# Kernel tuning notes

Hardware: AMD Instinct MI355X
Metric: run time of the kernel (lower is better)

The kernel has to match this reference:

```python
import jax, jax.numpy as jnp
import numpy as np

EMBED = 2048
HEADS = 16
B, T = 4, 2048


def setup_inputs() -> dict:
    key = jax.random.key(0)
    ks = jax.random.split(key, 8)
    s = 1.0 / np.sqrt(EMBED)
    return {
        "k": jax.random.normal(ks[0], (B, T, EMBED), dtype=jnp.float32),
        "q": jax.random.normal(ks[1], (B, T, EMBED), dtype=jnp.float32),
        "v": jax.random.normal(ks[2], (B, T, EMBED), dtype=jnp.float32),
        "Wk": jax.random.uniform(ks[3], (EMBED, EMBED), jnp.float32, -s, s),
        "Wq": jax.random.uniform(ks[4], (EMBED, EMBED), jnp.float32, -s, s),
        "Wv": jax.random.uniform(ks[5], (EMBED, EMBED), jnp.float32, -s, s),
        "Wo": jax.random.uniform(ks[6], (EMBED, EMBED), jnp.float32, -s, s),
        "bo": jax.random.uniform(ks[7], (EMBED,), jnp.float32, -s, s),
    }


def _split_heads(x):
    b, t, e = x.shape
    # 'b t (h n) -> b h t n'
    return x.reshape(b, t, HEADS, e // HEADS).transpose(0, 2, 1, 3)


def reference(k, q, v, Wk, Wq, Wv, Wo, bo):
    keys = _split_heads(k @ Wk.T)      # [b,h,t,n]
    queries = _split_heads(q @ Wq.T)
    values = _split_heads(v @ Wv.T)
    head_dim = queries.shape[-1]
    scale = 1.0 / jnp.sqrt(jnp.asarray(head_dim, queries.dtype))
    att = jnp.einsum('bhqn,bhkn->bhqk', queries, keys) * scale
    att = jax.nn.softmax(att, axis=-1)
    out = jnp.einsum('bhqk,bhkn->bhqn', att, values)  # [b,h,t,n]
    b, h, t, n = out.shape
    out = out.transpose(0, 2, 1, 3).reshape(b, t, h * n)  # 'b h t n -> b t (h n)'
    return out @ Wo.T + bo
```

## Files before the change

kernel.cpp:

```cpp
#include <hip/hip_runtime.h>


typedef __attribute__((ext_vector_type(4))) float f32x4;
typedef __attribute__((ext_vector_type(2))) float f32x2;
typedef __attribute__((ext_vector_type(8))) __bf16 bf16x8;
typedef __attribute__((ext_vector_type(4))) unsigned int u32x4;
typedef __attribute__((ext_vector_type(8))) unsigned short u16x8;
typedef __attribute__((ext_vector_type(4))) unsigned short u16x4;

#define DEVI static __device__ __forceinline__

DEVI unsigned short f2bf(float f) {
  union { float f; unsigned u; } x; x.f = f;
  unsigned u = x.u;
  return (unsigned short)((u + 0x7fffu + ((u >> 16) & 1u)) >> 16);
}
DEVI unsigned int pack2(float lo, float hi) {
  return (unsigned int)f2bf(lo) | ((unsigned int)f2bf(hi) << 16);
}
DEVI u32x4 pack8(const f32x4 a, const f32x4 b) {
  u32x4 r;
  r[0] = pack2(a[0], a[1]); r[1] = pack2(a[2], a[3]);
  r[2] = pack2(b[0], b[1]); r[3] = pack2(b[2], b[3]);
  return r;
}
DEVI void gload16(const unsigned short* g, unsigned short* l) {
  __builtin_amdgcn_global_load_lds(
      (const __attribute__((address_space(1))) unsigned int*)g,
      (__attribute__((address_space(3))) unsigned int*)l, 16, 0, 0);
}

template <int CTRL> DEVI float dppf(float x) {
  return __builtin_bit_cast(float, __builtin_amdgcn_update_dpp(
      __builtin_bit_cast(int, x), __builtin_bit_cast(int, x), CTRL, 0xF, 0xF, true));
}
DEVI float rowmax16(float x) {
  x = fmaxf(x, dppf<0x121>(x));
  x = fmaxf(x, dppf<0x122>(x));
  x = fmaxf(x, dppf<0x124>(x));
  x = fmaxf(x, dppf<0x128>(x));
  return x;
}
DEVI float rowsum16(float x) {
  x += dppf<0x121>(x);
  x += dppf<0x122>(x);
  x += dppf<0x124>(x);
  x += dppf<0x128>(x);
  return x;
}

__global__ __launch_bounds__(256) void convA(
    const float* __restrict__ q, const float* __restrict__ k,
    const float* __restrict__ v, unsigned short* __restrict__ dst)
{
  const int z = blockIdx.z;
  const float* src = z == 0 ? q : (z == 1 ? k : v);
  unsigned short* d = dst + (size_t)z * 16777216;
  size_t i = ((size_t)blockIdx.x * 256 + threadIdx.x) * 8;
  f32x4 a = *(const f32x4*)(src + i);
  f32x4 b = *(const f32x4*)(src + i + 4);
  *(u32x4*)(d + i) = pack8(a, b);
}

__global__ __launch_bounds__(256) void convW(
    const float* __restrict__ w0, const float* __restrict__ w1,
    const float* __restrict__ w2, const float* __restrict__ w3,
    unsigned short* __restrict__ dst)
{
  const int z = blockIdx.z;
  const float* src = z == 0 ? w0 : (z == 1 ? w1 : (z == 2 ? w2 : w3));
  unsigned short* d = dst + (size_t)z * 4194304;
  size_t i = ((size_t)blockIdx.x * 256 + threadIdx.x) * 8;
  f32x4 a = *(const f32x4*)(src + i);
  f32x4 b = *(const f32x4*)(src + i + 4);
  *(u32x4*)(d + i) = pack8(a, b);
}

#define STG2(gp, lp, tile) do { \
    gload16((gp) + (size_t)(tile) * 64,            (lp)); \
    gload16((gp) + (size_t)(tile) * 64 + 8 * 2048, (lp) + 8 * 64); \
  } while (0)
#define LDA8(bufoff, ksbit) { \
    _Pragma("unroll") for (int m = 0; m < 8; m++) \
      a[m] = *(const bf16x8*)(As + (bufoff) + (aoff[m] ^ (ksbit))); }
#define LDB2(bufoff, ksbit, n0) { \
    b0 = *(const bf16x8*)(Bs + (bufoff) + (boff[n0] ^ (ksbit))); \
    b1 = *(const bf16x8*)(Bs + (bufoff) + (boff[(n0) + 1] ^ (ksbit))); }
#define MM2(n0) { \
    __builtin_amdgcn_s_setprio(1); \
    _Pragma("unroll") for (int m = 0; m < 8; m++) { \
      acc[m][n0] = __builtin_amdgcn_mfma_f32_16x16x32_bf16(a[m], b0, acc[m][n0], 0, 0, 0); \
      acc[m][(n0) + 1] = __builtin_amdgcn_mfma_f32_16x16x32_bf16(a[m], b1, acc[m][(n0) + 1], 0, 0, 0); \
    } \
    __builtin_amdgcn_s_setprio(0); }
#define BARX() { __builtin_amdgcn_sched_barrier(0); __builtin_amdgcn_s_barrier(); }
#define WVM(n) asm volatile("s_waitcnt vmcnt(" #n ")" ::: "memory");

DEVI void gemm256_bf16(const unsigned short* __restrict__ A,
                       const unsigned short* __restrict__ Bm,
                       unsigned short* As, unsigned short* Bs,
                       int bm, int bn, int tid, f32x4 (&acc)[8][4])
{
  const int lane = tid & 63, w = tid >> 6;
  const int wm = w >> 2, wn = w & 3;
  const int sr = lane >> 3;
  const int sc = (lane & 7) ^ sr;
  const unsigned short* gA0 = A  + (size_t)(bm * 256 +   0 + w * 16 + sr) * 2048 + sc * 8;
  const unsigned short* gA1 = A  + (size_t)(bm * 256 + 128 + w * 16 + sr) * 2048 + sc * 8;
  const unsigned short* gB0 = Bm + (size_t)(bn * 256 +   0 + w * 16 + sr) * 2048 + sc * 8;
  const unsigned short* gB1 = Bm + (size_t)(bn * 256 + 128 + w * 16 + sr) * 2048 + sc * 8;
  unsigned short* lA00 = As +         (  0 + w * 16) * 64;
  unsigned short* lA01 = As +         (128 + w * 16) * 64;
  unsigned short* lA10 = As + 16384 + (  0 + w * 16) * 64;
  unsigned short* lA11 = As + 16384 + (128 + w * 16) * 64;
  unsigned short* lB00 = Bs +         (  0 + w * 16) * 64;
  unsigned short* lB01 = Bs +         (128 + w * 16) * 64;
  unsigned short* lB10 = Bs + 16384 + (  0 + w * 16) * 64;
  unsigned short* lB11 = Bs + 16384 + (128 + w * 16) * 64;

  const int fr = lane & 15, fk = lane >> 4;
  const int swz = (fk ^ (lane & 7)) << 3;
  int aoff[8], boff[4];
#pragma unroll
  for (int m = 0; m < 8; m++) aoff[m] = (wm * 128 + m * 16 + fr) * 64 + swz;
#pragma unroll
  for (int n = 0; n < 4; n++) boff[n] = (wn * 64 + n * 16 + fr) * 64 + swz;

  bf16x8 a[8], b0, b1;

  STG2(gA0, lA00, 0); STG2(gA1, lA01, 0); STG2(gB0, lB00, 0); STG2(gB1, lB01, 0);
  STG2(gA0, lA10, 1);
  WVM(2) BARX()

  for (int t = 0; t < 30; t += 2) {
    LDA8(0, 0) LDB2(0, 0, 0) STG2(gA1, lA11, t + 1);
    BARX() MM2(0) BARX()
    LDB2(0, 0, 2) STG2(gB0, lB10, t + 1);
    BARX() MM2(2) BARX()
    LDA8(0, 32) LDB2(0, 32, 0) STG2(gB1, lB11, t + 1);
    BARX() MM2(0) BARX()
    LDB2(0, 32, 2) STG2(gA0, lA00, t + 2);
    BARX() MM2(2) WVM(2) BARX()
    LDA8(16384, 0) LDB2(16384, 0, 0) STG2(gA1, lA01, t + 2);
    BARX() MM2(0) BARX()
    LDB2(16384, 0, 2) STG2(gB0, lB00, t + 2);
    BARX() MM2(2) BARX()
    LDA8(16384, 32) LDB2(16384, 32, 0) STG2(gB1, lB01, t + 2);
    BARX() MM2(0) BARX()
    LDB2(16384, 32, 2) STG2(gA0, lA10, t + 3);
    BARX() MM2(2) WVM(2) BARX()
  }
  LDA8(0, 0) LDB2(0, 0, 0) STG2(gA1, lA11, 31);
  BARX() MM2(0) BARX()
  LDB2(0, 0, 2) STG2(gB0, lB10, 31);
  BARX() MM2(2) BARX()
  LDA8(0, 32) LDB2(0, 32, 0) STG2(gB1, lB11, 31);
  BARX() MM2(0) BARX()
  LDB2(0, 32, 2)
  BARX() MM2(2) WVM(0) BARX()
  LDA8(16384, 0) LDB2(16384, 0, 0)
  BARX() MM2(0) BARX()
  LDB2(16384, 0, 2)
  BARX() MM2(2) BARX()
  LDA8(16384, 32) LDB2(16384, 32, 0)
  BARX() MM2(0) BARX()
  LDB2(16384, 32, 2)
  BARX() MM2(2)
}

DEVI int xcd_swz256(int bid) { return ((bid & 7) << 5) | (bid >> 3); }

__global__ __launch_bounds__(512, 2) void qkv_gemm_bf(
    const unsigned short* __restrict__ Abf, const unsigned short* __restrict__ Wbf,
    unsigned short* __restrict__ O0, unsigned short* __restrict__ O1,
    unsigned short* __restrict__ O2)
{
  __shared__ unsigned short As[2 * 256 * 64];
  __shared__ unsigned short Bs[2 * 256 * 64];
  const int z = blockIdx.z;
  const unsigned short* A = Abf + (size_t)z * 16777216;
  const unsigned short* W = Wbf + (size_t)z * 4194304;
  unsigned short* O = z == 0 ? O0 : (z == 1 ? O1 : O2);

  const int tid = threadIdx.x;
  const int lane = tid & 63, w = tid >> 6;
  const int wm = w >> 2, wn = w & 3;
  const int bs = xcd_swz256(blockIdx.x);
  const int bm = bs >> 3, bn = bs & 7;

  f32x4 acc[8][4];
#pragma unroll
  for (int m = 0; m < 8; m++)
#pragma unroll
    for (int n = 0; n < 4; n++) acc[m][n] = (f32x4)(0.0f);

  gemm256_bf16(A, W, As, Bs, bm, bn, tid, acc);

  const bool evenlane = (lane & 1) == 0;
#pragma unroll
  for (int m = 0; m < 8; m++) {
    int rowg = bm * 256 + wm * 128 + m * 16 + (lane >> 4) * 4;
#pragma unroll
    for (int n = 0; n < 4; n += 2) {
#pragma unroll
      for (int j = 0; j < 4; j++) {
        float v0 = acc[m][n][j], v1 = acc[m][n + 1][j];
        float p0 = __shfl_xor(v0, 1);
        float p1 = __shfl_xor(v1, 1);
        int row = rowg + j;
        int b = row >> 11, t = row & 2047;
        int colbase = bn * 256 + wn * 64;
        int col = evenlane ? (colbase + n * 16 + (lane & 15))
                           : (colbase + (n + 1) * 16 + (lane & 15) - 1);
        unsigned int wv = evenlane ? pack2(v0, p0) : pack2(p1, v1);
        int h = col >> 7, d = col & 127;
        *(unsigned int*)(O + (((size_t)(b * 16 + h) * 2048 + t) << 7) + d) = wv;
      }
    }
  }
}

__global__ __launch_bounds__(512, 2) void out_gemm_bf(
    const unsigned short* __restrict__ Ab, const unsigned short* __restrict__ Wb,
    const float* __restrict__ bias, float* __restrict__ Out)
{
  __shared__ unsigned short As[2 * 256 * 64];
  __shared__ unsigned short Bs[2 * 256 * 64];
  const int tid = threadIdx.x;
  const int lane = tid & 63, w = tid >> 6;
  const int wm = w >> 2, wn = w & 3;
  const int bs = xcd_swz256(blockIdx.x);
  const int bm = bs >> 3, bn = bs & 7;

  f32x4 acc[8][4];
#pragma unroll
  for (int m = 0; m < 8; m++)
#pragma unroll
    for (int n = 0; n < 4; n++) acc[m][n] = (f32x4)(0.0f);

  gemm256_bf16(Ab, Wb, As, Bs, bm, bn, tid, acc);

  float bv[4];
#pragma unroll
  for (int n = 0; n < 4; n++) bv[n] = bias[bn * 256 + wn * 64 + n * 16 + (lane & 15)];
  const bool evenlane = (lane & 1) == 0;
#pragma unroll
  for (int m = 0; m < 8; m++) {
    int rowg = bm * 256 + wm * 128 + m * 16 + (lane >> 4) * 4;
#pragma unroll
    for (int n = 0; n < 4; n += 2) {
#pragma unroll
      for (int j = 0; j < 4; j++) {
        float v0 = acc[m][n][j] + bv[n];
        float v1 = acc[m][n + 1][j] + bv[n + 1];
        float p0 = __shfl_xor(v0, 1);
        float p1 = __shfl_xor(v1, 1);
        int row = rowg + j;
        int colbase = bn * 256 + wn * 64;
        int col = evenlane ? (colbase + n * 16 + (lane & 15))
                           : (colbase + (n + 1) * 16 + (lane & 15) - 1);
        f32x2 wv;
        if (evenlane) { wv[0] = v0; wv[1] = p0; }
        else          { wv[0] = p1; wv[1] = v1; }
        *(f32x2*)(Out + (size_t)row * 2048 + col) = wv;
      }
    }
  }
}

__global__ __launch_bounds__(256) void qkv_gemm(
    const float* __restrict__ A0, const float* __restrict__ A1, const float* __restrict__ A2,
    const float* __restrict__ W0, const float* __restrict__ W1, const float* __restrict__ W2,
    unsigned short* __restrict__ O0, unsigned short* __restrict__ O1, unsigned short* __restrict__ O2)
{
  __shared__ unsigned short As[128 * 32];
  __shared__ unsigned short Bs[128 * 32];
  const int z = blockIdx.z;
  const float* A = z == 0 ? A0 : (z == 1 ? A1 : A2);
  const float* W = z == 0 ? W0 : (z == 1 ? W1 : W2);
  unsigned short* O = z == 0 ? O0 : (z == 1 ? O1 : O2);

  const int tid = threadIdx.x;
  const int lane = tid & 63;
  const int wave = tid >> 6;
  const int wm = wave >> 1, wn = wave & 1;
  const int bm = blockIdx.x >> 4, bn = blockIdx.x & 15;

  const int srow = tid >> 1;
  const int shalf = tid & 1;
  const float* Ap = A + (size_t)(bm * 128 + srow) * 2048 + shalf * 16;
  const float* Wp = W + (size_t)(bn * 128 + srow) * 2048 + shalf * 16;
  const int ssw = (srow >> 1) & 3;
  const int aoff0 = srow * 32 + (((shalf * 2 + 0) ^ ssw) << 3);
  const int aoff1 = srow * 32 + (((shalf * 2 + 1) ^ ssw) << 3);

  const int frow = lane & 15;
  const int fk = lane >> 4;

  f32x4 acc[4][4];
#pragma unroll
  for (int m = 0; m < 4; m++)
#pragma unroll
    for (int n = 0; n < 4; n++) acc[m][n] = (f32x4)(0.0f);

  for (int kk = 0; kk < 2048; kk += 32) {
    f32x4 a0 = *(const f32x4*)(Ap + kk);
    f32x4 a1 = *(const f32x4*)(Ap + kk + 4);
    f32x4 a2 = *(const f32x4*)(Ap + kk + 8);
    f32x4 a3 = *(const f32x4*)(Ap + kk + 12);
    f32x4 b0 = *(const f32x4*)(Wp + kk);
    f32x4 b1 = *(const f32x4*)(Wp + kk + 4);
    f32x4 b2 = *(const f32x4*)(Wp + kk + 8);
    f32x4 b3 = *(const f32x4*)(Wp + kk + 12);
    __syncthreads();
    *(u32x4*)(As + aoff0) = pack8(a0, a1);
    *(u32x4*)(As + aoff1) = pack8(a2, a3);
    *(u32x4*)(Bs + aoff0) = pack8(b0, b1);
    *(u32x4*)(Bs + aoff1) = pack8(b2, b3);
    __syncthreads();
    bf16x8 af[4], bfr[4];
#pragma unroll
    for (int m = 0; m < 4; m++) {
      int r = wm * 64 + m * 16 + frow;
      af[m] = *(const bf16x8*)(As + r * 32 + ((fk ^ ((r >> 1) & 3)) << 3));
    }
#pragma unroll
    for (int n = 0; n < 4; n++) {
      int r = wn * 64 + n * 16 + frow;
      bfr[n] = *(const bf16x8*)(Bs + r * 32 + ((fk ^ ((r >> 1) & 3)) << 3));
    }
#pragma unroll
    for (int m = 0; m < 4; m++)
#pragma unroll
      for (int n = 0; n < 4; n++)
        acc[m][n] = __builtin_amdgcn_mfma_f32_16x16x32_bf16(af[m], bfr[n], acc[m][n], 0, 0, 0);
  }

  const bool evenlane = (lane & 1) == 0;
#pragma unroll
  for (int m = 0; m < 4; m++) {
    int rowg = bm * 128 + wm * 64 + m * 16 + (lane >> 4) * 4;
#pragma unroll
    for (int n = 0; n < 4; n += 2) {
#pragma unroll
      for (int j = 0; j < 4; j++) {
        float v0 = acc[m][n][j], v1 = acc[m][n + 1][j];
        float p0 = __shfl_xor(v0, 1);
        float p1 = __shfl_xor(v1, 1);
        int row = rowg + j;
        int b = row >> 11, t = row & 2047;
        int colbase = bn * 128 + wn * 64;
        int col = evenlane ? (colbase + n * 16 + (lane & 15))
                           : (colbase + (n + 1) * 16 + (lane & 15) - 1);
        unsigned int wv = evenlane ? pack2(v0, p0) : pack2(p1, v1);
        int h = col >> 7, d = col & 127;
        *(unsigned int*)(O + (((size_t)(b * 16 + h) * 2048 + t) << 7) + d) = wv;
      }
    }
  }
}

__global__ __launch_bounds__(256, 2) void attn(
    const unsigned short* __restrict__ Qw, const unsigned short* __restrict__ Kw,
    const unsigned short* __restrict__ Vw, unsigned short* __restrict__ attout)
{
  __shared__ unsigned short Ks[2][64 * 128];
  __shared__ unsigned short Vs[2][128 * 64];
  __shared__ unsigned short Ps[128 * 64];

  const int bid = blockIdx.x;
  const int work = ((bid & 7) << 7) | (bid >> 3);
  const int bh = work >> 4;
  const int qtile = work & 15;
  const int b = bh >> 4, h = bh & 15;
  const unsigned short* Qbase = Qw + (size_t)bh * 2048 * 128 + qtile * 128 * 128;
  const unsigned short* Kbase = Kw + (size_t)bh * 2048 * 128;
  const unsigned short* Vbase = Vw + (size_t)bh * 2048 * 128;
  const int tid = threadIdx.x, lane = tid & 63, w = tid >> 6;
  const int frow = lane & 15, fk = lane >> 4;

  bf16x8 qf[2][4];
#pragma unroll
  for (int m = 0; m < 2; m++)
#pragma unroll
    for (int ks = 0; ks < 4; ks++)
      qf[m][ks] = *(const bf16x8*)(Qbase + (size_t)(w * 32 + m * 16 + frow) * 128 + ks * 32 + fk * 8);

  const int krow_i = lane >> 4;
  const int kslot = lane & 15;
  const int vkb = (tid & 7) * 8;
  const int vdb = (tid >> 3) * 4;

  f32x4 o[2][8];
#pragma unroll
  for (int m = 0; m < 2; m++)
#pragma unroll
    for (int n = 0; n < 8; n++) o[m][n] = (f32x4)(0.0f);
  float m_r[2][4], l_r[2][4];
#pragma unroll
  for (int m = 0; m < 2; m++)
#pragma unroll
    for (int j = 0; j < 4; j++) { m_r[m][j] = -INFINITY; l_r[m][j] = 0.f; }
  const float SC = 0.12751721769f;
  const float THR = 90.5f;

  {
#pragma unroll
    for (int i = 0; i < 4; i++) {
      int row = w * 16 + i * 4 + krow_i;
      gload16(Kbase + (size_t)row * 128 + ((kslot ^ (row & 15)) << 3),
              &Ks[0][(w * 16 + i * 4) * 128]);
    }
    u16x4 vr[8];
#pragma unroll
    for (int i = 0; i < 8; i++) vr[i] = *(const u16x4*)(Vbase + (size_t)(vkb + i) * 128 + vdb);
#pragma unroll
    for (int dd = 0; dd < 4; dd++) {
      int row = vdb + dd;
      u16x8 pk;
#pragma unroll
      for (int i = 0; i < 8; i++) pk[i] = vr[i][dd];
      *(u16x8*)((char*)&Vs[0][0] + row * 128 + (((tid & 7) ^ (row & 7)) << 4)) = pk;
    }
  }

  for (int kt = 0; kt < 32; kt++) {
    const int cur = kt & 1;
    __syncthreads();

    u16x4 vr[8];
    const bool have_next = (kt + 1) < 32;
    if (have_next) {
      const unsigned short* Kt = Kbase + (kt + 1) * 64 * 128;
      const unsigned short* Vt = Vbase + (kt + 1) * 64 * 128;
#pragma unroll
      for (int i = 0; i < 4; i++) {
        int row = w * 16 + i * 4 + krow_i;
        gload16(Kt + (size_t)row * 128 + ((kslot ^ (row & 15)) << 3),
                &Ks[cur ^ 1][(w * 16 + i * 4) * 128]);
      }
#pragma unroll
      for (int i = 0; i < 8; i++) vr[i] = *(const u16x4*)(Vt + (size_t)(vkb + i) * 128 + vdb);
    }

    f32x4 s[2][4];
#pragma unroll
    for (int m = 0; m < 2; m++)
#pragma unroll
      for (int n = 0; n < 4; n++) s[m][n] = (f32x4)(0.0f);
    __builtin_amdgcn_s_setprio(1);
#pragma unroll
    for (int ks = 0; ks < 4; ks++) {
#pragma unroll
      for (int n = 0; n < 4; n++) {
        int brow = n * 16 + frow;
        bf16x8 bk = *(const bf16x8*)(&Ks[cur][0] + brow * 128 + (((ks * 4 + fk) ^ (brow & 15)) << 3));
#pragma unroll
        for (int m = 0; m < 2; m++)
          s[m][n] = __builtin_amdgcn_mfma_f32_16x16x32_bf16(qf[m][ks], bk, s[m][n], 0, 0, 0);
      }
    }
    __builtin_amdgcn_s_setprio(0);

#pragma unroll
    for (int m = 0; m < 2; m++) {
#pragma unroll
      for (int j = 0; j < 4; j++) {
        float mx = fmaxf(fmaxf(s[m][0][j], s[m][1][j]), fmaxf(s[m][2][j], s[m][3][j]));
        mx = rowmax16(mx);
        float mo = m_r[m][j];
        if (!__all(mx - mo <= THR)) {
          float mnew = fmaxf(mo, mx);
          float f = __builtin_amdgcn_exp2f((mo - mnew) * SC);
          m_r[m][j] = mnew;
          l_r[m][j] *= f;
#pragma unroll
          for (int n = 0; n < 8; n++) o[m][n][j] *= f;
        }
        float mm = m_r[m][j];
        float psum = 0.f;
#pragma unroll
        for (int n = 0; n < 4; n++) {
          float p = __builtin_amdgcn_exp2f((s[m][n][j] - mm) * SC);
          s[m][n][j] = p;
          psum += p;
        }
        l_r[m][j] += rowsum16(psum);
      }
    }

#pragma unroll
    for (int m = 0; m < 2; m++) {
#pragma unroll
      for (int j = 0; j < 4; j++) {
        int row = w * 32 + m * 16 + (lane >> 4) * 4 + j;
        int swz = row & 7;
#pragma unroll
        for (int n = 0; n < 4; n++) {
          int col = (lane & 15) + 16 * n;
          *(unsigned short*)((char*)Ps + row * 128 + (((col >> 3) ^ swz) << 4) + (col & 7) * 2) =
              f2bf(s[m][n][j]);
        }
      }
    }

    __builtin_amdgcn_s_setprio(1);
#pragma unroll
    for (int ks = 0; ks < 2; ks++) {
      bf16x8 ap[2];
#pragma unroll
      for (int m = 0; m < 2; m++) {
        int arow = w * 32 + m * 16 + frow;
        ap[m] = *(const bf16x8*)((char*)Ps + arow * 128 + (((ks * 4 + fk) ^ (arow & 7)) << 4));
      }
#pragma unroll
      for (int n = 0; n < 8; n++) {
        int vrow = n * 16 + frow;
        bf16x8 bv = *(const bf16x8*)((char*)&Vs[cur][0] + vrow * 128 + (((ks * 4 + fk) ^ (vrow & 7)) << 4));
#pragma unroll
        for (int m = 0; m < 2; m++)
          o[m][n] = __builtin_amdgcn_mfma_f32_16x16x32_bf16(ap[m], bv, o[m][n], 0, 0, 0);
      }
    }
    __builtin_amdgcn_s_setprio(0);

    if (have_next) {
#pragma unroll
      for (int dd = 0; dd < 4; dd++) {
        int row = vdb + dd;
        u16x8 pk;
#pragma unroll
        for (int i = 0; i < 8; i++) pk[i] = vr[i][dd];
        *(u16x8*)((char*)&Vs[cur ^ 1][0] + row * 128 + (((tid & 7) ^ (row & 7)) << 4)) = pk;
      }
    }
  }

  const bool evenlane = (lane & 1) == 0;
#pragma unroll
  for (int m = 0; m < 2; m++) {
    float inv[4];
#pragma unroll
    for (int j = 0; j < 4; j++) inv[j] = 1.0f / l_r[m][j];
#pragma unroll
    for (int n = 0; n < 8; n += 2) {
#pragma unroll
      for (int j = 0; j < 4; j++) {
        float v0 = o[m][n][j] * inv[j], v1 = o[m][n + 1][j] * inv[j];
        float p0 = __shfl_xor(v0, 1);
        float p1 = __shfl_xor(v1, 1);
        int tq = qtile * 128 + w * 32 + m * 16 + (lane >> 4) * 4 + j;
        int col = evenlane ? (n * 16 + (lane & 15)) : ((n + 1) * 16 + (lane & 15) - 1);
        unsigned int wv = evenlane ? pack2(v0, p0) : pack2(p1, v1);
        *(unsigned int*)(attout + (size_t)(b * 2048 + tq) * 2048 + h * 128 + col) = wv;
      }
    }
  }
}

__global__ __launch_bounds__(256) void out_gemm(
    const unsigned short* __restrict__ Ab, const float* __restrict__ W,
    const float* __restrict__ bias, float* __restrict__ Out)
{
  __shared__ unsigned short As[128 * 32];
  __shared__ unsigned short Bs[128 * 32];

  const int tid = threadIdx.x;
  const int lane = tid & 63;
  const int wave = tid >> 6;
  const int wm = wave >> 1, wn = wave & 1;
  const int bm = blockIdx.x >> 4, bn = blockIdx.x & 15;

  const int srow = tid >> 1;
  const int shalf = tid & 1;
  const unsigned short* Ap = Ab + (size_t)(bm * 128 + srow) * 2048 + shalf * 16;
  const float* Wp = W + (size_t)(bn * 128 + srow) * 2048 + shalf * 16;
  const int ssw = (srow >> 1) & 3;
  const int aoff0 = srow * 32 + (((shalf * 2 + 0) ^ ssw) << 3);
  const int aoff1 = srow * 32 + (((shalf * 2 + 1) ^ ssw) << 3);

  const int frow = lane & 15;
  const int fk = lane >> 4;

  f32x4 acc[4][4];
#pragma unroll
  for (int m = 0; m < 4; m++)
#pragma unroll
    for (int n = 0; n < 4; n++) acc[m][n] = (f32x4)(0.0f);

  for (int kk = 0; kk < 2048; kk += 32) {
    u32x4 a0 = *(const u32x4*)(Ap + kk);
    u32x4 a1 = *(const u32x4*)(Ap + kk + 8);
    f32x4 b0 = *(const f32x4*)(Wp + kk);
    f32x4 b1 = *(const f32x4*)(Wp + kk + 4);
    f32x4 b2 = *(const f32x4*)(Wp + kk + 8);
    f32x4 b3 = *(const f32x4*)(Wp + kk + 12);
    __syncthreads();
    *(u32x4*)(As + aoff0) = a0;
    *(u32x4*)(As + aoff1) = a1;
    *(u32x4*)(Bs + aoff0) = pack8(b0, b1);
    *(u32x4*)(Bs + aoff1) = pack8(b2, b3);
    __syncthreads();
    bf16x8 af[4], bfr[4];
#pragma unroll
    for (int m = 0; m < 4; m++) {
      int r = wm * 64 + m * 16 + frow;
      af[m] = *(const bf16x8*)(As + r * 32 + ((fk ^ ((r >> 1) & 3)) << 3));
    }
#pragma unroll
    for (int n = 0; n < 4; n++) {
      int r = wn * 64 + n * 16 + frow;
      bfr[n] = *(const bf16x8*)(Bs + r * 32 + ((fk ^ ((r >> 1) & 3)) << 3));
    }
#pragma unroll
    for (int m = 0; m < 4; m++)
#pragma unroll
      for (int n = 0; n < 4; n++)
        acc[m][n] = __builtin_amdgcn_mfma_f32_16x16x32_bf16(af[m], bfr[n], acc[m][n], 0, 0, 0);
  }

  float bv[4];
#pragma unroll
  for (int n = 0; n < 4; n++) bv[n] = bias[bn * 128 + wn * 64 + n * 16 + (lane & 15)];
  const bool evenlane = (lane & 1) == 0;
#pragma unroll
  for (int m = 0; m < 4; m++) {
    int rowg = bm * 128 + wm * 64 + m * 16 + (lane >> 4) * 4;
#pragma unroll
    for (int n = 0; n < 4; n += 2) {
#pragma unroll
      for (int j = 0; j < 4; j++) {
        float v0 = acc[m][n][j] + bv[n];
        float v1 = acc[m][n + 1][j] + bv[n + 1];
        float p0 = __shfl_xor(v0, 1);
        float p1 = __shfl_xor(v1, 1);
        int row = rowg + j;
        int colbase = bn * 128 + wn * 64;
        int col = evenlane ? (colbase + n * 16 + (lane & 15))
                           : (colbase + (n + 1) * 16 + (lane & 15) - 1);
        f32x2 wv;
        if (evenlane) { wv[0] = v0; wv[1] = p0; }
        else          { wv[0] = p1; wv[1] = v1; }
        *(f32x2*)(Out + (size_t)row * 2048 + col) = wv;
      }
    }
  }
}

extern "C" void kernel_launch(void* const* d_in, const int* in_sizes, int n_in,
                              void* d_out, int out_size, void* d_ws, size_t ws_size,
                              hipStream_t stream)
{
  const float* k  = (const float*)d_in[0];
  const float* q  = (const float*)d_in[1];
  const float* v  = (const float*)d_in[2];
  const float* Wk = (const float*)d_in[3];
  const float* Wq = (const float*)d_in[4];
  const float* Wv = (const float*)d_in[5];
  const float* Wo = (const float*)d_in[6];
  const float* bo = (const float*)d_in[7];
  float* out = (float*)d_out;

  const size_t HSZ = (size_t)4 * 16 * 2048 * 128;

  if (ws_size >= (size_t)224 << 20) {
    unsigned short* Abf = (unsigned short*)d_ws;
    unsigned short* Wbf = Abf + 3 * HSZ;
    unsigned short* Qw  = Wbf + 4 * 4194304;
    unsigned short* Kw  = Qw + HSZ;
    unsigned short* Vw  = Kw + HSZ;
    unsigned short* Aw  = Abf;

    convA<<<dim3(8192, 1, 3), 256, 0, stream>>>(q, k, v, Abf);
    convW<<<dim3(2048, 1, 4), 256, 0, stream>>>(Wq, Wk, Wv, Wo, Wbf);
    qkv_gemm_bf<<<dim3(256, 1, 3), 512, 0, stream>>>(Abf, Wbf, Qw, Kw, Vw);
    attn<<<dim3(1024), 256, 0, stream>>>(Qw, Kw, Vw, Aw);
    out_gemm_bf<<<dim3(256), 512, 0, stream>>>(Aw, Wbf + 3 * 4194304, bo, out);
  } else {
    unsigned short* Qw = (unsigned short*)d_ws;
    unsigned short* Kw = Qw + HSZ;
    unsigned short* Vw = Kw + HSZ;
    unsigned short* Aw = Vw + HSZ;
    qkv_gemm<<<dim3(1024, 1, 3), 256, 0, stream>>>(q, k, v, Wq, Wk, Wv, Qw, Kw, Vw);
    attn<<<dim3(1024), 256, 0, stream>>>(Qw, Kw, Vw, Aw);
    out_gemm<<<dim3(1024), 256, 0, stream>>>(Aw, Wo, bo, out);
  }
}
```

Before: 565.8 us.

## Store V projection transposed and load it into LDS with async copies

The V projection GEMM epilogue now writes its output transposed per head ([b,h,d,t]). The attention kernel can then fill the V tile in shared memory with direct global-to-LDS loads, replacing the register gather and in-register transpose with deferred stores. The P tile is also packed two bf16 values at a time using a DPP lane swap and v_cvt_pk_bf16_f32, which halves the LDS store count. This removes VGPR pressure and VALU work from the attention loop. The cost is that the transposed epilogue writes are strided by 2048 and less coalesced.

```diff
diff --git a/kernel.cpp b/kernel.cpp
--- a/kernel.cpp
+++ b/kernel.cpp
@@ -5,8 +5,7 @@
 typedef __attribute__((ext_vector_type(2))) float f32x2;
 typedef __attribute__((ext_vector_type(8))) __bf16 bf16x8;
 typedef __attribute__((ext_vector_type(4))) unsigned int u32x4;
-typedef __attribute__((ext_vector_type(8))) unsigned short u16x8;
-typedef __attribute__((ext_vector_type(4))) unsigned short u16x4;
+typedef __attribute__((ext_vector_type(2))) unsigned int u32x2;
 
 #define DEVI static __device__ __forceinline__
 
@@ -196,6 +195,24 @@
 
   gemm256_bf16(A, W, As, Bs, bm, bn, tid, acc);
 
+  if (z == 2) {
+#pragma unroll
+    for (int m = 0; m < 8; m++) {
+      int rowg = bm * 256 + wm * 128 + m * 16 + (lane >> 4) * 4;
+      int bb = rowg >> 11, t0 = rowg & 2047;
+#pragma unroll
+      for (int n = 0; n < 4; n++) {
+        int col = bn * 256 + wn * 64 + n * 16 + (lane & 15);
+        int hh = col >> 7, dd = col & 127;
+        u32x2 wv;
+        wv[0] = pack2(acc[m][n][0], acc[m][n][1]);
+        wv[1] = pack2(acc[m][n][2], acc[m][n][3]);
+        *(u32x2*)(O + (((size_t)(bb * 16 + hh) * 128 + dd) << 11) + t0) = wv;
+      }
+    }
+    return;
+  }
+
   const bool evenlane = (lane & 1) == 0;
 #pragma unroll
   for (int m = 0; m < 8; m++) {
@@ -336,6 +353,24 @@
         acc[m][n] = __builtin_amdgcn_mfma_f32_16x16x32_bf16(af[m], bfr[n], acc[m][n], 0, 0, 0);
   }
 
+  if (z == 2) {
+#pragma unroll
+    for (int m = 0; m < 4; m++) {
+      int rowg = bm * 128 + wm * 64 + m * 16 + (lane >> 4) * 4;
+      int bb = rowg >> 11, t0 = rowg & 2047;
+#pragma unroll
+      for (int n = 0; n < 4; n++) {
+        int col = bn * 128 + wn * 64 + n * 16 + (lane & 15);
+        int hh = col >> 7, dd = col & 127;
+        u32x2 wv;
+        wv[0] = pack2(acc[m][n][0], acc[m][n][1]);
+        wv[1] = pack2(acc[m][n][2], acc[m][n][3]);
+        *(u32x2*)(O + (((size_t)(bb * 16 + hh) * 128 + dd) << 11) + t0) = wv;
+      }
+    }
+    return;
+  }
+
   const bool evenlane = (lane & 1) == 0;
 #pragma unroll
   for (int m = 0; m < 4; m++) {
@@ -362,7 +397,7 @@
 
 __global__ __launch_bounds__(256, 2) void attn(
     const unsigned short* __restrict__ Qw, const unsigned short* __restrict__ Kw,
-    const unsigned short* __restrict__ Vw, unsigned short* __restrict__ attout)
+    const unsigned short* __restrict__ VwT, unsigned short* __restrict__ attout)
 {
   __shared__ unsigned short Ks[2][64 * 128];
   __shared__ unsigned short Vs[2][128 * 64];
@@ -375,7 +410,7 @@
   const int b = bh >> 4, h = bh & 15;
   const unsigned short* Qbase = Qw + (size_t)bh * 2048 * 128 + qtile * 128 * 128;
   const unsigned short* Kbase = Kw + (size_t)bh * 2048 * 128;
-  const unsigned short* Vbase = Vw + (size_t)bh * 2048 * 128;
+  const unsigned short* VbaseT = VwT + (size_t)bh * 2048 * 128;
   const int tid = threadIdx.x, lane = tid & 63, w = tid >> 6;
   const int frow = lane & 15, fk = lane >> 4;
 
@@ -388,8 +423,8 @@
 
   const int krow_i = lane >> 4;
   const int kslot = lane & 15;
-  const int vkb = (tid & 7) * 8;
-  const int vdb = (tid >> 3) * 4;
+  const int vrow_i = lane >> 3;
+  const int vslot = (lane & 7) ^ vrow_i;
 
   f32x4 o[2][8];
 #pragma unroll
@@ -411,16 +446,11 @@
       gload16(Kbase + (size_t)row * 128 + ((kslot ^ (row & 15)) << 3),
               &Ks[0][(w * 16 + i * 4) * 128]);
     }
-    u16x4 vr[8];
-#pragma unroll
-    for (int i = 0; i < 8; i++) vr[i] = *(const u16x4*)(Vbase + (size_t)(vkb + i) * 128 + vdb);
-#pragma unroll
-    for (int dd = 0; dd < 4; dd++) {
-      int row = vdb + dd;
-      u16x8 pk;
-#pragma unroll
-      for (int i = 0; i < 8; i++) pk[i] = vr[i][dd];
-      *(u16x8*)((char*)&Vs[0][0] + row * 128 + (((tid & 7) ^ (row & 7)) << 4)) = pk;
+#pragma unroll
+    for (int i = 0; i < 4; i++) {
+      int d = w * 32 + i * 8 + vrow_i;
+      gload16(VbaseT + (size_t)d * 2048 + vslot * 8,
+              &Vs[0][(w * 32 + i * 8) * 64]);
     }
   }
 
@@ -428,11 +458,9 @@
     const int cur = kt & 1;
     __syncthreads();
 
-    u16x4 vr[8];
     const bool have_next = (kt + 1) < 32;
     if (have_next) {
       const unsigned short* Kt = Kbase + (kt + 1) * 64 * 128;
-      const unsigned short* Vt = Vbase + (kt + 1) * 64 * 128;
 #pragma unroll
       for (int i = 0; i < 4; i++) {
         int row = w * 16 + i * 4 + krow_i;
@@ -440,7 +468,11 @@
                 &Ks[cur ^ 1][(w * 16 + i * 4) * 128]);
       }
 #pragma unroll
-      for (int i = 0; i < 8; i++) vr[i] = *(const u16x4*)(Vt + (size_t)(vkb + i) * 128 + vdb);
+      for (int i = 0; i < 4; i++) {
+        int d = w * 32 + i * 8 + vrow_i;
+        gload16(VbaseT + (size_t)d * 2048 + (kt + 1) * 64 + vslot * 8,
+                &Vs[cur ^ 1][(w * 32 + i * 8) * 64]);
+      }
     }
 
     f32x4 s[2][4];
@@ -486,20 +518,24 @@
           psum += p;
         }
         l_r[m][j] += rowsum16(psum);
-      }
-    }
-
-#pragma unroll
-    for (int m = 0; m < 2; m++) {
-#pragma unroll
-      for (int j = 0; j < 4; j++) {
+
         int row = w * 32 + m * 16 + (lane >> 4) * 4 + j;
-        int swz = row & 7;
+        int swzp = row & 7;
+        unsigned prv[4];
 #pragma unroll
         for (int n = 0; n < 4; n++) {
-          int col = (lane & 15) + 16 * n;
-          *(unsigned short*)((char*)Ps + row * 128 + (((col >> 3) ^ swz) << 4) + (col & 7) * 2) =
-              f2bf(s[m][n][j]);
+          float p = s[m][n][j];
+          float ph = dppf<0xB1>(p);
+          unsigned pr;
+          asm("v_cvt_pk_bf16_f32 %0, %1, %2" : "=v"(pr) : "v"(p), "v"(ph));
+          prv[n] = pr;
+        }
+        if (!(lane & 1)) {
+#pragma unroll
+          for (int n = 0; n < 4; n++) {
+            int col = frow + 16 * n;
+            *(unsigned*)((char*)Ps + row * 128 + (((col >> 3) ^ swzp) << 4) + (col & 7) * 2) = prv[n];
+          }
         }
       }
     }
@@ -523,17 +559,6 @@
       }
     }
     __builtin_amdgcn_s_setprio(0);
-
-    if (have_next) {
-#pragma unroll
-      for (int dd = 0; dd < 4; dd++) {
-        int row = vdb + dd;
-        u16x8 pk;
-#pragma unroll
-        for (int i = 0; i < 8; i++) pk[i] = vr[i][dd];
-        *(u16x8*)((char*)&Vs[cur ^ 1][0] + row * 128 + (((tid & 7) ^ (row & 7)) << 4)) = pk;
-      }
-    }
   }
 
   const bool evenlane = (lane & 1) == 0;
```

Result: no change. 556.0 us (-1.7%).
